# Optimization experiments

Hardware: AMD Instinct MI355X
Metric: run time of the kernel (lower is better)

Reference implementation:

```python
import jax, jax.numpy as jnp
import numpy as np

B, T, D_IN, H, E = 256, 512, 256, 256, 96  # batch, enc seq, input_size, hidden_size, num_embeddings


def setup_inputs() -> dict:
    key = jax.random.key(0)
    ks = jax.random.split(key, 12)
    s = 0.05
    return {
        "prev_h": jax.random.normal(ks[0], (B, H), jnp.float32),
        "prev_c": jax.random.normal(ks[1], (B, H), jnp.float32),
        "batch_H": jax.random.normal(ks[2], (B, T, D_IN), jnp.float32),
        "char_onehots": jax.random.uniform(ks[3], (B, E), jnp.float32),
        "W_i2h": jax.random.normal(ks[4], (H, D_IN), jnp.float32) * s,
        "W_h2h": jax.random.normal(ks[5], (H, H), jnp.float32) * s,
        "b_h2h": jax.random.normal(ks[6], (H,), jnp.float32) * s,
        "W_score": jax.random.normal(ks[7], (1, H), jnp.float32) * s,
        "W_ih": jax.random.normal(ks[8], (4 * H, D_IN + E), jnp.float32) * s,
        "W_hh": jax.random.normal(ks[9], (4 * H, H), jnp.float32) * s,
        "b_ih": jax.random.normal(ks[10], (4 * H,), jnp.float32) * s,
        "b_hh": jax.random.normal(ks[11], (4 * H,), jnp.float32) * s,
    }


def reference(prev_h, prev_c, batch_H, char_onehots,
              W_i2h, W_h2h, b_h2h, W_score, W_ih, W_hh, b_ih, b_hh):
    # additive attention over encoder features
    proj = jnp.einsum('btd,hd->bth', batch_H, W_i2h)          # [B,T,H]
    hid = prev_h @ W_h2h.T + b_h2h                             # [B,H]
    e = jnp.einsum('bth,oh->bto', jnp.tanh(proj + hid[:, None, :]), W_score)  # [B,T,1]
    alpha = jax.nn.softmax(e, axis=1)                          # [B,T,1]
    context = jnp.einsum('bt,btd->bd', alpha[..., 0], batch_H) # [B,D_IN]
    x = jnp.concatenate([context, char_onehots], axis=1)       # [B,D_IN+E]
    # LSTM cell step (PyTorch gate order: i, f, g, o)
    gates = x @ W_ih.T + b_ih + prev_h @ W_hh.T + b_hh         # [B,4H]
    i, f, g, o = jnp.split(gates, 4, axis=1)
    c_new = jax.nn.sigmoid(f) * prev_c + jax.nn.sigmoid(i) * jnp.tanh(g)
    h_new = jax.nn.sigmoid(o) * jnp.tanh(c_new)
    return (h_new, c_new, jnp.swapaxes(alpha, 1, 2))           # alpha -> [B,1,T]
```

## Files before the change

kernel.cpp:

```cpp
#include <hip/hip_runtime.h>

typedef __attribute__((ext_vector_type(8))) short short8;
typedef __attribute__((ext_vector_type(4))) float f32x4;

#define KPAD 40

#define WS_HID    0u
#define WS_E      262144u
#define WS_CTX    786432u
#define WS_WBF    1048576u
#define WS_WCAT   1212416u

__device__ __forceinline__ unsigned f2bfu(float f) {
    union { float f; unsigned u; } v; v.f = f;
    return (v.u + 0x7FFFu + ((v.u >> 16) & 1u)) >> 16;
}
__device__ __forceinline__ float tanh_fast(float x) {
    float e2 = __expf(2.f * x);
    return 1.f - 2.f * __builtin_amdgcn_rcpf(e2 + 1.f);
}
__device__ __forceinline__ float sigmoid_fast(float x) {
    return __builtin_amdgcn_rcpf(1.f + __expf(-x));
}

__global__ __launch_bounds__(256) void k_prep(
    const float* __restrict__ prev_h, const float* __restrict__ W_i2h,
    const float* __restrict__ W_h2h, const float* __restrict__ b_h2h,
    const float* __restrict__ W_ih,  const float* __restrict__ W_hh,
    float* __restrict__ hid, short* __restrict__ Wbf, short* __restrict__ Wcat)
{
    int bid = blockIdx.x, tid = threadIdx.x;
    if (bid < 256) {
        __shared__ float ph[256];
        ph[tid] = prev_h[bid * 256 + tid];
        __syncthreads();
        float acc = b_h2h[tid];
        const float4* w = (const float4*)(W_h2h + tid * 256);
        #pragma unroll 8
        for (int k4 = 0; k4 < 64; ++k4) {
            float4 ww = w[k4];
            acc += ww.x * ph[k4*4+0] + ww.y * ph[k4*4+1] + ww.z * ph[k4*4+2] + ww.w * ph[k4*4+3];
        }
        hid[bid * 256 + tid] = acc;
    } else if (bid < 576) {
        int idx = (bid - 256) * 256 + tid;
        int kc = idx / (256 * KPAD);
        int rem = idx % (256 * KPAD);
        int n = rem / KPAD, kk = rem % KPAD;
        float v = (kk < 32) ? W_i2h[n * 256 + kc * 32 + kk] : 0.f;
        Wbf[idx] = (short)f2bfu(v);
    } else {
        int idx = (bid - 576) * 256 + tid;
        int kc = idx / (1024 * KPAD);
        int rem = idx % (1024 * KPAD);
        int np = rem / KPAD, kk = rem % KPAD;
        int h = np >> 2, g = np & 3;
        float v = 0.f;
        if (kk < 32) {
            int k = kc * 32 + kk;
            if (k < 352) v = W_ih[(g * 256 + h) * 352 + k];
            else         v = W_hh[(g * 256 + h) * 256 + (k - 352)];
        }
        Wcat[idx] = (short)f2bfu(v);
    }
}

__global__ __launch_bounds__(256, 3) void k_escore(
    const float* __restrict__ BH, const short* __restrict__ Wbf,
    const float* __restrict__ hid, const float* __restrict__ Wsc,
    float* __restrict__ e_out)
{
    __shared__ short Al[2][64 * KPAD];
    __shared__ short Bl[2][256 * KPAD];
    __shared__ float eps[4][64];

    const int tid = threadIdx.x;
    const int lane = tid & 63;
    const int w = tid >> 6;
    const int l15 = lane & 15, lg = lane >> 4;
    const int bt0 = blockIdx.x * 64;
    const int b = bt0 >> 9;

    const int arow = tid >> 2, akg = tid & 3;
    const float* asrc = BH + (size_t)(bt0 + arow) * 256 + akg * 8;

    f32x4 acc[4][4];
    #pragma unroll
    for (int i = 0; i < 4; i++)
        #pragma unroll
        for (int j = 0; j < 4; j++) acc[i][j] = (f32x4){0.f, 0.f, 0.f, 0.f};

    auto stage = [&](int kc, int bu) {
        float4 x0 = *(const float4*)(asrc + kc * 32);
        float4 x1 = *(const float4*)(asrc + kc * 32 + 4);
        int4 p;
        p.x = (int)((f2bfu(x0.y) << 16) | f2bfu(x0.x));
        p.y = (int)((f2bfu(x0.w) << 16) | f2bfu(x0.z));
        p.z = (int)((f2bfu(x1.y) << 16) | f2bfu(x1.x));
        p.w = (int)((f2bfu(x1.w) << 16) | f2bfu(x1.z));
        *(int4*)&Al[bu][arow * KPAD + akg * 8] = p;
        const int4* bs = (const int4*)(Wbf + (size_t)(kc * 256 + tid) * KPAD);
        int4* bd = (int4*)&Bl[bu][tid * KPAD];
        #pragma unroll
        for (int i = 0; i < 5; i++) bd[i] = bs[i];
    };

    stage(0, 0);
    __syncthreads();

    for (int ks = 0; ks < 8; ++ks) {
        int cur = ks & 1;
        short8 af[4], bf_[4];
        #pragma unroll
        for (int rf = 0; rf < 4; rf++)
            af[rf] = *(const short8*)&Al[cur][(rf * 16 + l15) * KPAD + lg * 8];
        #pragma unroll
        for (int cf = 0; cf < 4; cf++)
            bf_[cf] = *(const short8*)&Bl[cur][(w * 64 + cf * 16 + l15) * KPAD + lg * 8];
        if (ks < 7) stage(ks + 1, cur ^ 1);
        #pragma unroll
        for (int rf = 0; rf < 4; rf++)
            #pragma unroll
            for (int cf = 0; cf < 4; cf++)
                acc[rf][cf] = __builtin_amdgcn_mfma_f32_16x16x32_bf16(af[rf], bf_[cf], acc[rf][cf], 0, 0, 0);
        __syncthreads();
    }

    float esum[4][4];
    #pragma unroll
    for (int rf = 0; rf < 4; rf++)
        #pragma unroll
        for (int r = 0; r < 4; r++) esum[rf][r] = 0.f;

    #pragma unroll
    for (int cf = 0; cf < 4; cf++) {
        int col = w * 64 + cf * 16 + l15;
        float wsv = Wsc[col];
        float hd = hid[b * 256 + col];
        #pragma unroll
        for (int rf = 0; rf < 4; rf++)
            #pragma unroll
            for (int r = 0; r < 4; r++)
                esum[rf][r] += wsv * tanh_fast(acc[rf][cf][r] + hd);
    }
    #pragma unroll
    for (int rf = 0; rf < 4; rf++)
        #pragma unroll
        for (int r = 0; r < 4; r++) {
            float s = esum[rf][r];
            s += __shfl_xor(s, 1); s += __shfl_xor(s, 2);
            s += __shfl_xor(s, 4); s += __shfl_xor(s, 8);
            esum[rf][r] = s;
        }
    if (l15 == 0) {
        #pragma unroll
        for (int rf = 0; rf < 4; rf++)
            #pragma unroll
            for (int r = 0; r < 4; r++)
                eps[w][rf * 16 + lg * 4 + r] = esum[rf][r];
    }
    __syncthreads();
    if (tid < 64)
        e_out[bt0 + tid] = eps[0][tid] + eps[1][tid] + eps[2][tid] + eps[3][tid];
}

__global__ __launch_bounds__(256) void k_smctx(
    const float* __restrict__ e, const float* __restrict__ BH,
    float* __restrict__ alpha_out, float* __restrict__ ctx)
{
    __shared__ float al[512];
    __shared__ float r1[4], r2[4];
    int b = blockIdx.x, t = threadIdx.x;
    float v0 = e[b * 512 + t], v1 = e[b * 512 + 256 + t];
    float m = fmaxf(v0, v1);
    #pragma unroll
    for (int off = 32; off; off >>= 1) m = fmaxf(m, __shfl_xor(m, off));
    if ((t & 63) == 0) r1[t >> 6] = m;
    __syncthreads();
    m = fmaxf(fmaxf(r1[0], r1[1]), fmaxf(r1[2], r1[3]));
    float a0 = __expf(v0 - m), a1 = __expf(v1 - m);
    float s = a0 + a1;
    #pragma unroll
    for (int off = 32; off; off >>= 1) s += __shfl_xor(s, off);
    if ((t & 63) == 0) r2[t >> 6] = s;
    __syncthreads();
    s = r2[0] + r2[1] + r2[2] + r2[3];
    float inv = 1.f / s;
    a0 *= inv; a1 *= inv;
    alpha_out[b * 512 + t] = a0;
    alpha_out[b * 512 + 256 + t] = a1;
    al[t] = a0; al[256 + t] = a1;
    __syncthreads();
    const float* bh = BH + (size_t)b * 512 * 256 + t;
    float acc = 0.f;
    #pragma unroll 16
    for (int tt = 0; tt < 512; ++tt) acc += al[tt] * bh[(size_t)tt * 256];
    ctx[b * 256 + t] = acc;
}

__global__ __launch_bounds__(256) void k_gates_lstm(
    const float* __restrict__ ctx, const float* __restrict__ onehot,
    const float* __restrict__ prev_h, const short* __restrict__ Wcat,
    const float* __restrict__ b_ih, const float* __restrict__ b_hh,
    const float* __restrict__ prev_c, float* __restrict__ out)
{
    __shared__ char smem[20800];
    short* AlB = (short*)smem;
    short* BlB = (short*)smem + 5120;
    const int tid = threadIdx.x;
    const int lane = tid & 63;
    const int w = tid >> 6;
    const int l15 = lane & 15, lg = lane >> 4;
    const int rb = blockIdx.x * 64;
    const int hb = blockIdx.y;

    f32x4 acc[4];
    #pragma unroll
    for (int j = 0; j < 4; j++) acc[j] = (f32x4){0.f, 0.f, 0.f, 0.f};

    const int arow = tid >> 2, akg = tid & 3;
    const int rg = rb + arow;

    auto stageAB = [&](int kc, int bu) {
        int k0 = kc * 32 + akg * 8;
        const float4* p;
        if (k0 < 256)      p = (const float4*)(ctx    + rg * 256 + k0);
        else if (k0 < 352) p = (const float4*)(onehot + rg * 96  + (k0 - 256));
        else               p = (const float4*)(prev_h + rg * 256 + (k0 - 352));
        float4 x0 = p[0], x1 = p[1];
        int4 q;
        q.x = (int)((f2bfu(x0.y) << 16) | f2bfu(x0.x));
        q.y = (int)((f2bfu(x0.w) << 16) | f2bfu(x0.z));
        q.z = (int)((f2bfu(x1.y) << 16) | f2bfu(x1.x));
        q.w = (int)((f2bfu(x1.w) << 16) | f2bfu(x1.z));
        *(int4*)&AlB[bu * 2560 + arow * KPAD + akg * 8] = q;
        {
            int u = tid;
            int n = u / 5, i = u % 5;
            ((int4*)&BlB[bu * 2560 + n * KPAD])[i] =
                ((const int4*)(Wcat + ((size_t)kc * 1024 + hb * 64 + n) * KPAD))[i];
        }
        if (tid < 64) {
            int u = tid + 256;
            int n = u / 5, i = u % 5;
            ((int4*)&BlB[bu * 2560 + n * KPAD])[i] =
                ((const int4*)(Wcat + ((size_t)kc * 1024 + hb * 64 + n) * KPAD))[i];
        }
    };

    stageAB(0, 0);
    __syncthreads();

    for (int kc = 0; kc < 19; ++kc) {
        int cur = kc & 1;
        short8 af = *(const short8*)&AlB[cur * 2560 + (w * 16 + l15) * KPAD + lg * 8];
        short8 bf_[4];
        #pragma unroll
        for (int cf = 0; cf < 4; cf++)
            bf_[cf] = *(const short8*)&BlB[cur * 2560 + (cf * 16 + l15) * KPAD + lg * 8];
        if (kc < 18) stageAB(kc + 1, cur ^ 1);
        #pragma unroll
        for (int cf = 0; cf < 4; cf++)
            acc[cf] = __builtin_amdgcn_mfma_f32_16x16x32_bf16(af, bf_[cf], acc[cf], 0, 0, 0);
        __syncthreads();
    }

    float* Gt = (float*)smem;
    #pragma unroll
    for (int cf = 0; cf < 4; cf++) {
        int col = cf * 16 + l15;
        int np = hb * 64 + col;
        int hg = np >> 2, g = np & 3;
        float bias = b_ih[g * 256 + hg] + b_hh[g * 256 + hg];
        #pragma unroll
        for (int r = 0; r < 4; r++)
            Gt[(w * 16 + lg * 4 + r) * 65 + col] = acc[cf][r] + bias;
    }
    __syncthreads();

    #pragma unroll
    for (int it = 0; it < 4; ++it) {
        int elem = it * 256 + tid;
        int row = elem >> 4, hl = elem & 15;
        float gi = Gt[row * 65 + hl * 4 + 0];
        float gf = Gt[row * 65 + hl * 4 + 1];
        float gg = Gt[row * 65 + hl * 4 + 2];
        float go = Gt[row * 65 + hl * 4 + 3];
        int bg = rb + row, hglob = hb * 16 + hl;
        float c = sigmoid_fast(gf) * prev_c[bg * 256 + hglob] + sigmoid_fast(gi) * tanh_fast(gg);
        out[bg * 256 + hglob] = sigmoid_fast(go) * tanh_fast(c);
        out[65536 + bg * 256 + hglob] = c;
    }
}

extern "C" void kernel_launch(void* const* d_in, const int* in_sizes, int n_in,
                              void* d_out, int out_size, void* d_ws, size_t ws_size,
                              hipStream_t stream) {
    (void)in_sizes; (void)n_in; (void)out_size; (void)ws_size;
    const float* prev_h  = (const float*)d_in[0];
    const float* prev_c  = (const float*)d_in[1];
    const float* batch_H = (const float*)d_in[2];
    const float* onehot  = (const float*)d_in[3];
    const float* W_i2h   = (const float*)d_in[4];
    const float* W_h2h   = (const float*)d_in[5];
    const float* b_h2h   = (const float*)d_in[6];
    const float* W_score = (const float*)d_in[7];
    const float* W_ih    = (const float*)d_in[8];
    const float* W_hh    = (const float*)d_in[9];
    const float* b_ih    = (const float*)d_in[10];
    const float* b_hh    = (const float*)d_in[11];

    char* ws = (char*)d_ws;
    float* hid   = (float*)(ws + WS_HID);
    float* e     = (float*)(ws + WS_E);
    float* ctx   = (float*)(ws + WS_CTX);
    short* Wbf   = (short*)(ws + WS_WBF);
    short* Wcat  = (short*)(ws + WS_WCAT);

    float* out = (float*)d_out;
    float* alpha = out + 131072;

    hipLaunchKernelGGL(k_prep,       dim3(3616),   dim3(256), 0, stream,
                       prev_h, W_i2h, W_h2h, b_h2h, W_ih, W_hh, hid, Wbf, Wcat);
    hipLaunchKernelGGL(k_escore,     dim3(2048),   dim3(256), 0, stream,
                       batch_H, Wbf, hid, W_score, e);
    hipLaunchKernelGGL(k_smctx,      dim3(256),    dim3(256), 0, stream,
                       e, batch_H, alpha, ctx);
    hipLaunchKernelGGL(k_gates_lstm, dim3(4, 16),  dim3(256), 0, stream,
                       ctx, onehot, prev_h, Wcat, b_ih, b_hh, prev_c, out);
}
```

Before: 91.73 us.

## Fuse softmax-context into score kernel, keep bf16 tile resident, drop Wcat prep

The score kernel now keeps all 8 K-chunks of the bf16 batch_H tile in LDS and reuses it to compute unnormalized exp weights and per-chunk partial context sums. This removes the second full fp32 read of batch_H in the softmax/context kernel. A small finalize kernel then normalizes alpha and sums the partial contexts. The gates kernel converts W_ih/W_hh to bf16 on the fly instead of using a prep-converted Wcat. Risks: the softmax skips max subtraction, so large scores could overflow. The context is built from bf16-rounded batch_H. LDS use rises to 80KB, which lowers occupancy to 2 blocks.

```diff
diff --git a/kernel.cpp b/kernel.cpp
--- a/kernel.cpp
+++ b/kernel.cpp
@@ -6,15 +6,20 @@
 #define KPAD 40
 
 #define WS_HID    0u
-#define WS_E      262144u
-#define WS_CTX    786432u
-#define WS_WBF    1048576u
-#define WS_WCAT   1212416u
+#define WS_P      262144u
+#define WS_Z      786432u
+#define WS_CTX    794624u
+#define WS_CTXP   1056768u
+#define WS_WBF    3153920u
 
 __device__ __forceinline__ unsigned f2bfu(float f) {
     union { float f; unsigned u; } v; v.f = f;
     return (v.u + 0x7FFFu + ((v.u >> 16) & 1u)) >> 16;
 }
+__device__ __forceinline__ float bf2f(short s) {
+    union { float f; unsigned u; } v; v.u = ((unsigned)(unsigned short)s) << 16;
+    return v.f;
+}
 __device__ __forceinline__ float tanh_fast(float x) {
     float e2 = __expf(2.f * x);
     return 1.f - 2.f * __builtin_amdgcn_rcpf(e2 + 1.f);
@@ -22,12 +27,19 @@
 __device__ __forceinline__ float sigmoid_fast(float x) {
     return __builtin_amdgcn_rcpf(1.f + __expf(-x));
 }
+__device__ __forceinline__ int4 pack8(float4 x0, float4 x1) {
+    int4 q;
+    q.x = (int)((f2bfu(x0.y) << 16) | f2bfu(x0.x));
+    q.y = (int)((f2bfu(x0.w) << 16) | f2bfu(x0.z));
+    q.z = (int)((f2bfu(x1.y) << 16) | f2bfu(x1.x));
+    q.w = (int)((f2bfu(x1.w) << 16) | f2bfu(x1.z));
+    return q;
+}
 
 __global__ __launch_bounds__(256) void k_prep(
     const float* __restrict__ prev_h, const float* __restrict__ W_i2h,
     const float* __restrict__ W_h2h, const float* __restrict__ b_h2h,
-    const float* __restrict__ W_ih,  const float* __restrict__ W_hh,
-    float* __restrict__ hid, short* __restrict__ Wbf, short* __restrict__ Wcat)
+    float* __restrict__ hid, short* __restrict__ Wbf)
 {
     int bid = blockIdx.x, tid = threadIdx.x;
     if (bid < 256) {
@@ -42,37 +54,27 @@
             acc += ww.x * ph[k4*4+0] + ww.y * ph[k4*4+1] + ww.z * ph[k4*4+2] + ww.w * ph[k4*4+3];
         }
         hid[bid * 256 + tid] = acc;
-    } else if (bid < 576) {
+    } else {
         int idx = (bid - 256) * 256 + tid;
         int kc = idx / (256 * KPAD);
         int rem = idx % (256 * KPAD);
         int n = rem / KPAD, kk = rem % KPAD;
         float v = (kk < 32) ? W_i2h[n * 256 + kc * 32 + kk] : 0.f;
         Wbf[idx] = (short)f2bfu(v);
-    } else {
-        int idx = (bid - 576) * 256 + tid;
-        int kc = idx / (1024 * KPAD);
-        int rem = idx % (1024 * KPAD);
-        int np = rem / KPAD, kk = rem % KPAD;
-        int h = np >> 2, g = np & 3;
-        float v = 0.f;
-        if (kk < 32) {
-            int k = kc * 32 + kk;
-            if (k < 352) v = W_ih[(g * 256 + h) * 352 + k];
-            else         v = W_hh[(g * 256 + h) * 256 + (k - 352)];
-        }
-        Wcat[idx] = (short)f2bfu(v);
-    }
-}
-
-__global__ __launch_bounds__(256, 3) void k_escore(
+    }
+}
+
+__global__ __launch_bounds__(256, 2) void k_escore_ctx(
     const float* __restrict__ BH, const short* __restrict__ Wbf,
     const float* __restrict__ hid, const float* __restrict__ Wsc,
-    float* __restrict__ e_out)
+    float* __restrict__ p_out, float* __restrict__ zbuf, float* __restrict__ ctxp)
 {
-    __shared__ short Al[2][64 * KPAD];
-    __shared__ short Bl[2][256 * KPAD];
-    __shared__ float eps[4][64];
+    __shared__ char smem[81920];
+    short* Al = (short*)smem;
+    short* Bl = (short*)(smem + 40960);
+    float* eps = (float*)(smem + 40960);
+    float* pl  = (float*)(smem + 41984);
+    float* r8  = (float*)(smem + 42240);
 
     const int tid = threadIdx.x;
     const int lane = tid & 63;
@@ -80,6 +82,7 @@
     const int l15 = lane & 15, lg = lane >> 4;
     const int bt0 = blockIdx.x * 64;
     const int b = bt0 >> 9;
+    const int c = (bt0 >> 6) & 7;
 
     const int arow = tid >> 2, akg = tid & 3;
     const float* asrc = BH + (size_t)(bt0 + arow) * 256 + akg * 8;
@@ -90,34 +93,28 @@
         #pragma unroll
         for (int j = 0; j < 4; j++) acc[i][j] = (f32x4){0.f, 0.f, 0.f, 0.f};
 
-    auto stage = [&](int kc, int bu) {
+    auto stage = [&](int kc) {
         float4 x0 = *(const float4*)(asrc + kc * 32);
         float4 x1 = *(const float4*)(asrc + kc * 32 + 4);
-        int4 p;
-        p.x = (int)((f2bfu(x0.y) << 16) | f2bfu(x0.x));
-        p.y = (int)((f2bfu(x0.w) << 16) | f2bfu(x0.z));
-        p.z = (int)((f2bfu(x1.y) << 16) | f2bfu(x1.x));
-        p.w = (int)((f2bfu(x1.w) << 16) | f2bfu(x1.z));
-        *(int4*)&Al[bu][arow * KPAD + akg * 8] = p;
+        *(int4*)&Al[kc * 2560 + arow * KPAD + akg * 8] = pack8(x0, x1);
         const int4* bs = (const int4*)(Wbf + (size_t)(kc * 256 + tid) * KPAD);
-        int4* bd = (int4*)&Bl[bu][tid * KPAD];
+        int4* bd = (int4*)&Bl[(kc & 1) * 10240 + tid * KPAD];
         #pragma unroll
         for (int i = 0; i < 5; i++) bd[i] = bs[i];
     };
 
-    stage(0, 0);
+    stage(0);
     __syncthreads();
 
     for (int ks = 0; ks < 8; ++ks) {
-        int cur = ks & 1;
         short8 af[4], bf_[4];
         #pragma unroll
         for (int rf = 0; rf < 4; rf++)
-            af[rf] = *(const short8*)&Al[cur][(rf * 16 + l15) * KPAD + lg * 8];
+            af[rf] = *(const short8*)&Al[ks * 2560 + (rf * 16 + l15) * KPAD + lg * 8];
         #pragma unroll
         for (int cf = 0; cf < 4; cf++)
-            bf_[cf] = *(const short8*)&Bl[cur][(w * 64 + cf * 16 + l15) * KPAD + lg * 8];
-        if (ks < 7) stage(ks + 1, cur ^ 1);
+            bf_[cf] = *(const short8*)&Bl[(ks & 1) * 10240 + (w * 64 + cf * 16 + l15) * KPAD + lg * 8];
+        if (ks < 7) stage(ks + 1);
         #pragma unroll
         for (int rf = 0; rf < 4; rf++)
             #pragma unroll
@@ -157,52 +154,70 @@
         for (int rf = 0; rf < 4; rf++)
             #pragma unroll
             for (int r = 0; r < 4; r++)
-                eps[w][rf * 16 + lg * 4 + r] = esum[rf][r];
-    }
-    __syncthreads();
-    if (tid < 64)
-        e_out[bt0 + tid] = eps[0][tid] + eps[1][tid] + eps[2][tid] + eps[3][tid];
-}
-
-__global__ __launch_bounds__(256) void k_smctx(
-    const float* __restrict__ e, const float* __restrict__ BH,
-    float* __restrict__ alpha_out, float* __restrict__ ctx)
+                eps[w * 64 + rf * 16 + lg * 4 + r] = esum[rf][r];
+    }
+    __syncthreads();
+
+    if (tid < 64) {
+        float e = eps[tid] + eps[64 + tid] + eps[128 + tid] + eps[192 + tid];
+        float p = __expf(e);
+        p_out[bt0 + tid] = p;
+        pl[tid] = p;
+        float z = p;
+        z += __shfl_xor(z, 1); z += __shfl_xor(z, 2); z += __shfl_xor(z, 4);
+        z += __shfl_xor(z, 8); z += __shfl_xor(z, 16); z += __shfl_xor(z, 32);
+        if (tid == 0) zbuf[blockIdx.x] = z;
+    }
+    __syncthreads();
+
+    {
+        int tg = tid & 7, dg = tid >> 3;
+        int d0 = dg * 8;
+        int kc = d0 >> 5, dd = d0 & 31;
+        float a8[8] = {0.f,0.f,0.f,0.f,0.f,0.f,0.f,0.f};
+        #pragma unroll
+        for (int tt = 0; tt < 8; ++tt) {
+            int t = tt * 8 + tg;
+            short8 v = *(const short8*)&Al[kc * 2560 + t * KPAD + dd];
+            float pv = pl[t];
+            #pragma unroll
+            for (int j = 0; j < 8; ++j) a8[j] += pv * bf2f(v[j]);
+        }
+        #pragma unroll
+        for (int j = 0; j < 8; ++j) r8[tg * 256 + d0 + j] = a8[j];
+    }
+    __syncthreads();
+    {
+        float s = 0.f;
+        #pragma unroll
+        for (int g = 0; g < 8; ++g) s += r8[g * 256 + tid];
+        ctxp[((size_t)(c * 256 + b)) * 256 + tid] = s;
+    }
+}
+
+__global__ __launch_bounds__(256) void k_finalize(
+    const float* __restrict__ p, const float* __restrict__ zbuf,
+    const float* __restrict__ ctxp, float* __restrict__ alpha, float* __restrict__ ctx)
 {
-    __shared__ float al[512];
-    __shared__ float r1[4], r2[4];
     int b = blockIdx.x, t = threadIdx.x;
-    float v0 = e[b * 512 + t], v1 = e[b * 512 + 256 + t];
-    float m = fmaxf(v0, v1);
-    #pragma unroll
-    for (int off = 32; off; off >>= 1) m = fmaxf(m, __shfl_xor(m, off));
-    if ((t & 63) == 0) r1[t >> 6] = m;
-    __syncthreads();
-    m = fmaxf(fmaxf(r1[0], r1[1]), fmaxf(r1[2], r1[3]));
-    float a0 = __expf(v0 - m), a1 = __expf(v1 - m);
-    float s = a0 + a1;
-    #pragma unroll
-    for (int off = 32; off; off >>= 1) s += __shfl_xor(s, off);
-    if ((t & 63) == 0) r2[t >> 6] = s;
-    __syncthreads();
-    s = r2[0] + r2[1] + r2[2] + r2[3];
-    float inv = 1.f / s;
-    a0 *= inv; a1 *= inv;
-    alpha_out[b * 512 + t] = a0;
-    alpha_out[b * 512 + 256 + t] = a1;
-    al[t] = a0; al[256 + t] = a1;
-    __syncthreads();
-    const float* bh = BH + (size_t)b * 512 * 256 + t;
-    float acc = 0.f;
-    #pragma unroll 16
-    for (int tt = 0; tt < 512; ++tt) acc += al[tt] * bh[(size_t)tt * 256];
-    ctx[b * 256 + t] = acc;
+    float Z = 0.f;
+    #pragma unroll
+    for (int cc = 0; cc < 8; ++cc) Z += zbuf[b * 8 + cc];
+    float inv = 1.f / Z;
+    alpha[b * 512 + t] = p[b * 512 + t] * inv;
+    alpha[b * 512 + 256 + t] = p[b * 512 + 256 + t] * inv;
+    float s = 0.f;
+    #pragma unroll
+    for (int cc = 0; cc < 8; ++cc) s += ctxp[((size_t)(cc * 256 + b)) * 256 + t];
+    ctx[b * 256 + t] = s * inv;
 }
 
 __global__ __launch_bounds__(256) void k_gates_lstm(
     const float* __restrict__ ctx, const float* __restrict__ onehot,
-    const float* __restrict__ prev_h, const short* __restrict__ Wcat,
-    const float* __restrict__ b_ih, const float* __restrict__ b_hh,
-    const float* __restrict__ prev_c, float* __restrict__ out)
+    const float* __restrict__ prev_h, const float* __restrict__ W_ih,
+    const float* __restrict__ W_hh, const float* __restrict__ b_ih,
+    const float* __restrict__ b_hh, const float* __restrict__ prev_c,
+    float* __restrict__ out)
 {
     __shared__ char smem[20800];
     short* AlB = (short*)smem;
@@ -220,32 +235,23 @@
 
     const int arow = tid >> 2, akg = tid & 3;
     const int rg = rb + arow;
+    const int bn = tid >> 2, bq = tid & 3;
+    const int np_ = hb * 64 + bn, hh_ = np_ >> 2, gg_ = np_ & 3;
+    const float* wih_row = W_ih + (size_t)(gg_ * 256 + hh_) * 352;
+    const float* whh_row = W_hh + (size_t)(gg_ * 256 + hh_) * 256;
 
     auto stageAB = [&](int kc, int bu) {
         int k0 = kc * 32 + akg * 8;
-        const float4* p;
-        if (k0 < 256)      p = (const float4*)(ctx    + rg * 256 + k0);
-        else if (k0 < 352) p = (const float4*)(onehot + rg * 96  + (k0 - 256));
-        else               p = (const float4*)(prev_h + rg * 256 + (k0 - 352));
-        float4 x0 = p[0], x1 = p[1];
-        int4 q;
-        q.x = (int)((f2bfu(x0.y) << 16) | f2bfu(x0.x));
-        q.y = (int)((f2bfu(x0.w) << 16) | f2bfu(x0.z));
-        q.z = (int)((f2bfu(x1.y) << 16) | f2bfu(x1.x));
-        q.w = (int)((f2bfu(x1.w) << 16) | f2bfu(x1.z));
-        *(int4*)&AlB[bu * 2560 + arow * KPAD + akg * 8] = q;
-        {
-            int u = tid;
-            int n = u / 5, i = u % 5;
-            ((int4*)&BlB[bu * 2560 + n * KPAD])[i] =
-                ((const int4*)(Wcat + ((size_t)kc * 1024 + hb * 64 + n) * KPAD))[i];
-        }
-        if (tid < 64) {
-            int u = tid + 256;
-            int n = u / 5, i = u % 5;
-            ((int4*)&BlB[bu * 2560 + n * KPAD])[i] =
-                ((const int4*)(Wcat + ((size_t)kc * 1024 + hb * 64 + n) * KPAD))[i];
-        }
+        const float4* pa;
+        if (k0 < 256)      pa = (const float4*)(ctx    + rg * 256 + k0);
+        else if (k0 < 352) pa = (const float4*)(onehot + rg * 96  + (k0 - 256));
+        else               pa = (const float4*)(prev_h + rg * 256 + (k0 - 352));
+        float4 x0 = pa[0], x1 = pa[1];
+        *(int4*)&AlB[bu * 2560 + arow * KPAD + akg * 8] = pack8(x0, x1);
+        int kb = kc * 32 + bq * 8;
+        const float* pb = (kb < 352) ? (wih_row + kb) : (whh_row + (kb - 352));
+        float4 y0 = *(const float4*)pb, y1 = *(const float4*)(pb + 4);
+        *(int4*)&BlB[bu * 2560 + bn * KPAD + bq * 8] = pack8(y0, y1);
     };
 
     stageAB(0, 0);
@@ -287,9 +293,9 @@
         float gg = Gt[row * 65 + hl * 4 + 2];
         float go = Gt[row * 65 + hl * 4 + 3];
         int bg = rb + row, hglob = hb * 16 + hl;
-        float c = sigmoid_fast(gf) * prev_c[bg * 256 + hglob] + sigmoid_fast(gi) * tanh_fast(gg);
-        out[bg * 256 + hglob] = sigmoid_fast(go) * tanh_fast(c);
-        out[65536 + bg * 256 + hglob] = c;
+        float cv = sigmoid_fast(gf) * prev_c[bg * 256 + hglob] + sigmoid_fast(gi) * tanh_fast(gg);
+        out[bg * 256 + hglob] = sigmoid_fast(go) * tanh_fast(cv);
+        out[65536 + bg * 256 + hglob] = cv;
     }
 }
 
@@ -312,20 +318,21 @@
 
     char* ws = (char*)d_ws;
     float* hid   = (float*)(ws + WS_HID);
-    float* e     = (float*)(ws + WS_E);
+    float* p     = (float*)(ws + WS_P);
+    float* zbuf  = (float*)(ws + WS_Z);
     float* ctx   = (float*)(ws + WS_CTX);
+    float* ctxp  = (float*)(ws + WS_CTXP);
     short* Wbf   = (short*)(ws + WS_WBF);
-    short* Wcat  = (short*)(ws + WS_WCAT);
 
     float* out = (float*)d_out;
     float* alpha = out + 131072;
 
-    hipLaunchKernelGGL(k_prep,       dim3(3616),   dim3(256), 0, stream,
-                       prev_h, W_i2h, W_h2h, b_h2h, W_ih, W_hh, hid, Wbf, Wcat);
-    hipLaunchKernelGGL(k_escore,     dim3(2048),   dim3(256), 0, stream,
-                       batch_H, Wbf, hid, W_score, e);
-    hipLaunchKernelGGL(k_smctx,      dim3(256),    dim3(256), 0, stream,
-                       e, batch_H, alpha, ctx);
+    hipLaunchKernelGGL(k_prep,       dim3(576),    dim3(256), 0, stream,
+                       prev_h, W_i2h, W_h2h, b_h2h, hid, Wbf);
+    hipLaunchKernelGGL(k_escore_ctx, dim3(2048),   dim3(256), 0, stream,
+                       batch_H, Wbf, hid, W_score, p, zbuf, ctxp);
+    hipLaunchKernelGGL(k_finalize,   dim3(256),    dim3(256), 0, stream,
+                       p, zbuf, ctxp, alpha, ctx);
     hipLaunchKernelGGL(k_gates_lstm, dim3(4, 16),  dim3(256), 0, stream,
-                       ctx, onehot, prev_h, Wcat, b_ih, b_hh, prev_c, out);
-}
+                       ctx, onehot, prev_h, W_ih, W_hh, b_ih, b_hh, prev_c, out);
+}
```

After: 79.33 us. 13.5% less time.
